# Kernel tuning notes

Measured on AMD Instinct MI355X. Metric: run time of the kernel, lower is better.

Reference implementation:

```python
import jax, jax.numpy as jnp
import numpy as np

MARGIN = 0.2
NEG_INF = -1e30


def setup_inputs() -> dict:
    key = jax.random.key(0)
    k1, k2 = jax.random.split(key)
    B, D, C = 384, 256, 48
    features = jax.random.normal(k1, (B, D), dtype=jnp.float32)
    labels = jax.random.randint(k2, (B,), 0, C, dtype=jnp.int32)
    return {"features": features, "labels": labels, "epoch": 5}


def reference(features, labels, epoch):
    B = features.shape[0]
    # pairwise euclidean distance, clamped like torch.clamp(min=1e-11)
    diff = features[:, None, :] - features[None, :, :]          # [B,B,D]
    dist = jnp.sqrt(jnp.clip(jnp.sum(diff * diff, axis=-1), 1e-11))  # [B,B]

    idx = jnp.arange(B)
    same = labels[:, None] == labels[None, :]
    pos_mask = same & (idx[None, :] > idx[:, None])             # pairs (i,j), j>i, same label
    neg_mask = ~same

    # Gumbel-max sampling replaces the per-row np.random.choice host loop.
    gumbel = jax.random.gumbel(jax.random.key(42), (B, B, B), dtype=dist.dtype)

    if epoch > 3:
        # semi-hard negatives: pos_dist < d(i,k) < pos_dist + margin, weights 1/d(i,k)
        d_ik = dist[:, None, :]                                 # [B,1,B]
        d_pos = dist[:, :, None]                                # [B,B,1]
        semi = neg_mask[:, None, :] & (d_ik > d_pos) & (d_ik < d_pos + MARGIN)  # [B,B,B]
        logits = jnp.where(semi, -jnp.log(dist)[:, None, :], NEG_INF)  # log(1/d)
        has_neg = jnp.any(semi, axis=-1)                        # [B,B]
    else:
        # uniform random negative per (i,j) pair
        logits = jnp.where(neg_mask[:, None, :], 0.0, NEG_INF)  # [B,1,B]
        has_neg = jnp.broadcast_to(jnp.any(neg_mask, axis=-1)[:, None], (B, B))

    neg_idx = jnp.argmax(logits + gumbel, axis=-1)              # [B,B]
    neg_dist = jnp.take_along_axis(dist, neg_idx, axis=1)       # d(i, sampled_neg)

    valid = pos_mask & has_neg
    # MarginRankingLoss(neg, pos, target=1) = relu(pos - neg + margin)
    per_pair = jax.nn.relu(dist - neg_dist + MARGIN)
    count = jnp.sum(valid)
    total = jnp.sum(jnp.where(valid, per_pair, 0.0))
    return jnp.where(count > 0, total / jnp.maximum(count, 1), 0.0)
```

## Files before the change

kernel.cpp:

```cpp
#include <hip/hip_runtime.h>
#include <hip/hip_bf16.h>
#include <stdint.h>

#define BSZ 384
#define DD  256
#define NWAVES 6
#define NEG_BIG -3.0e38f
#define DONE_BASE 0xAAAAAAAAu

__device__ __forceinline__ void threefry_0_42(uint32_t c0, uint32_t c1,
                                              uint32_t& o0, uint32_t& o1) {
    const uint32_t k0 = 0u;
    const uint32_t k1 = 42u;
    const uint32_t k2 = 0u ^ 42u ^ 0x1BD11BDAu;
    uint32_t x0 = c0 + k0;
    uint32_t x1 = c1 + k1;
#define TF_RND(R) { x0 += x1; x1 = (x1 << (R)) | (x1 >> (32 - (R))); x1 ^= x0; }
    TF_RND(13) TF_RND(15) TF_RND(26) TF_RND(6)
    x0 += k1; x1 += k2 + 1u;
    TF_RND(17) TF_RND(29) TF_RND(16) TF_RND(24)
    x0 += k2; x1 += k0 + 2u;
    TF_RND(13) TF_RND(15) TF_RND(26) TF_RND(6)
    x0 += k0; x1 += k1 + 3u;
    TF_RND(17) TF_RND(29) TF_RND(16) TF_RND(24)
    x0 += k1; x1 += k2 + 4u;
    TF_RND(13) TF_RND(15) TF_RND(26) TF_RND(6)
    x0 += k2; x1 += k0 + 5u;
#undef TF_RND
    o0 = x0; o1 = x1;
}

__device__ __forceinline__ float gumbel_at(uint32_t idx) {
    uint32_t r0, r1;
    threefry_0_42(0u, idx, r0, r1);
    uint32_t bits = r0 ^ r1;
    uint32_t mant = bits >> 9;
    float f = __uint_as_float(mant | 0x3F800000u) - 1.0f;
    float u = (mant == 0u) ? 1.17549435e-38f : f;
    return -logf(-logf(u));
}

__global__ __launch_bounds__(BSZ) void fused_kernel(const float* __restrict__ F,
                                                    const int* __restrict__ labels,
                                                    const int* __restrict__ epochp,
                                                    float* __restrict__ tot_slot,
                                                    unsigned int* __restrict__ cnt_slot,
                                                    unsigned int* __restrict__ done,
                                                    float* __restrict__ out) {
    __shared__ float    row[BSZ];
    __shared__ float    nlog[BSZ];
    __shared__ int      slab[BSZ];
    __shared__ int      plist[BSZ];
    __shared__ int      npos;
    __shared__ int      is_last;
    __shared__ float    wtot[NWAVES];
    __shared__ unsigned wcnt[NWAVES];

    const int i    = blockIdx.x;
    const int tid  = threadIdx.x;
    const int wave = tid >> 6;
    const int lane = tid & 63;
    const int rl   = lane >> 3;
    const int s    = lane & 7;

    slab[tid] = labels[tid];
    if (tid == 0) npos = 0;
    __syncthreads();

    const int lab_i = slab[i];
    if (tid > i && slab[tid] == lab_i)
        plist[atomicAdd(&npos, 1)] = tid;
    const int  epoch   = *epochp;
    const bool semisel = (epoch > 3);
    __syncthreads();

    const int np = npos;
    float    t_total = 0.0f;
    unsigned t_count = 0u;

    if (np > 0) {
        const float4* F4 = (const float4*)F;

        float4 fi[8];
#pragma unroll
        for (int t = 0; t < 8; ++t) fi[t] = F4[i * (DD / 4) + t * 8 + s];

        for (int c = 0; c < 8; ++c) {
            const int k = c * 48 + wave * 8 + rl;
            const float4* fk = F4 + (size_t)k * (DD / 4);
            float a0 = 0.f, a1 = 0.f, a2 = 0.f, a3 = 0.f;
#pragma unroll
            for (int t = 0; t < 8; ++t) {
                float4 b = fk[t * 8 + s];
                float d0 = fi[t].x - b.x;
                float d1 = fi[t].y - b.y;
                float d2 = fi[t].z - b.z;
                float d3 = fi[t].w - b.w;
                a0 = fmaf(d0, d0, a0);
                a1 = fmaf(d1, d1, a1);
                a2 = fmaf(d2, d2, a2);
                a3 = fmaf(d3, d3, a3);
            }
            float p = (a0 + a1) + (a2 + a3);
            p += __shfl_down(p, 4, 64);
            p += __shfl_down(p, 2, 64);
            p += __shfl_down(p, 1, 64);
            if (s == 0) row[k] = sqrtf(fmaxf(p, 1e-11f));
        }
        __syncthreads();
        nlog[tid] = semisel ? -logf(row[tid]) : 0.0f;
        __syncthreads();

        for (int p = wave; p < np; p += NWAVES) {
            const int   j     = plist[p];
            const float d_pos = row[j];
            const float hi    = d_pos + 0.2f;
            float v  = NEG_BIG;
            int   kk = 0;
#pragma unroll
            for (int c = 0; c < BSZ / 64; ++c) {
                const int   k   = c * 64 + lane;
                const float dkk = row[k];
                const bool cand = (slab[k] != lab_i) &&
                                  (!semisel || (dkk > d_pos && dkk < hi));
                if (__any(cand)) {
                    if (cand) {
                        const uint32_t idx = (uint32_t)(i * BSZ + j) * (uint32_t)BSZ
                                             + (uint32_t)k;
                        float val = nlog[k] + gumbel_at(idx);
                        if (val > v) { v = val; kk = k; }
                    }
                }
            }
#pragma unroll
            for (int off = 32; off; off >>= 1) {
                float ov = __shfl_down(v, off, 64);
                int   oi = __shfl_down(kk, off, 64);
                if (ov > v || (ov == v && oi < kk)) { v = ov; kk = oi; }
            }
            if (lane == 0 && v > -1.0e38f) {
                t_total += fmaxf(d_pos - row[kk] + 0.2f, 0.0f);
                t_count += 1u;
            }
        }
    }

    if (lane == 0) { wtot[wave] = t_total; wcnt[wave] = t_count; }
    __syncthreads();
    if (tid == 0) {
        float    tt = 0.0f;
        unsigned cc = 0u;
#pragma unroll
        for (int q = 0; q < NWAVES; ++q) { tt += wtot[q]; cc += wcnt[q]; }
        atomicExch(&tot_slot[i], tt);
        atomicExch(&cnt_slot[i], cc);
        __threadfence();
        const unsigned prev = atomicAdd(done, 1u);
        is_last = (prev == DONE_BASE + (unsigned)(BSZ - 1)) ? 1 : 0;
    }
    __syncthreads();

    if (is_last) {
        float    t = atomicAdd(&tot_slot[tid], 0.0f);
        unsigned c = atomicAdd(&cnt_slot[tid], 0u);
#pragma unroll
        for (int off = 32; off; off >>= 1) {
            t += __shfl_down(t, off, 64);
            c += __shfl_down(c, off, 64);
        }
        if (lane == 0) { wtot[wave] = t; wcnt[wave] = c; }
        __syncthreads();
        if (tid == 0) {
            float    tt = 0.0f;
            unsigned cc = 0u;
#pragma unroll
            for (int q = 0; q < NWAVES; ++q) { tt += wtot[q]; cc += wcnt[q]; }
            out[0] = (cc > 0u) ? (tt / (float)cc) : 0.0f;
        }
    }
}

extern "C" void kernel_launch(void* const* d_in, const int* in_sizes, int n_in,
                              void* d_out, int out_size, void* d_ws, size_t ws_size,
                              hipStream_t stream) {
    const float* F      = (const float*)d_in[0];
    const int*   labels = (const int*)d_in[1];
    const int*   epoch  = (const int*)d_in[2];
    float*       out    = (float*)d_out;

    if (ws_size < (2 * BSZ + 1) * sizeof(float)) return;
    float*        tot_slot = (float*)d_ws;
    unsigned int* cnt_slot = (unsigned int*)d_ws + BSZ;
    unsigned int* done     = (unsigned int*)d_ws + 2 * BSZ;

    fused_kernel<<<BSZ, BSZ, 0, stream>>>(F, labels, epoch,
                                          tot_slot, cnt_slot, done, out);
}
```

Before: 72.17 us.

## Pair early and late anchor rows per block to cut grid to 256 blocks

The grid shrinks from 384 to 256 blocks. The first 128 blocks each handle two anchor rows, b and 256+b, so a row with many positive pairs is paired with one that has few. The distance phase computes both rows in one pass, reusing each loaded feature row, and the positive-pair lists of both anchors share one tagged worklist. This aims to balance work across the CUs in a single wave of blocks and to cut redundant feature loads, at the cost of extra registers and per-pair indirection.

```diff
diff --git a/kernel.cpp b/kernel.cpp
--- a/kernel.cpp
+++ b/kernel.cpp
@@ -4,6 +4,8 @@
 
 #define BSZ 384
 #define DD  256
+#define NBLK 256
+#define NDUAL (BSZ - NBLK)
 #define NWAVES 6
 #define NEG_BIG -3.0e38f
 #define DONE_BASE 0xAAAAAAAAu
@@ -47,29 +49,36 @@
                                                     unsigned int* __restrict__ cnt_slot,
                                                     unsigned int* __restrict__ done,
                                                     float* __restrict__ out) {
-    __shared__ float    row[BSZ];
-    __shared__ float    nlog[BSZ];
+    __shared__ float    row[2][BSZ];
+    __shared__ float    nlg[2][BSZ];
     __shared__ int      slab[BSZ];
-    __shared__ int      plist[BSZ];
+    __shared__ int      plist[512];
     __shared__ int      npos;
     __shared__ int      is_last;
     __shared__ float    wtot[NWAVES];
     __shared__ unsigned wcnt[NWAVES];
 
-    const int i    = blockIdx.x;
+    const int b    = blockIdx.x;
     const int tid  = threadIdx.x;
     const int wave = tid >> 6;
     const int lane = tid & 63;
     const int rl   = lane >> 3;
     const int s    = lane & 7;
 
+    const int  i0   = b;
+    const bool dual = (b < NDUAL);
+    const int  i1   = dual ? (NBLK + b) : 0;
+
     slab[tid] = labels[tid];
     if (tid == 0) npos = 0;
     __syncthreads();
 
-    const int lab_i = slab[i];
-    if (tid > i && slab[tid] == lab_i)
+    const int lab0 = slab[i0];
+    const int lab1 = dual ? slab[i1] : -1;
+    if (tid > i0 && slab[tid] == lab0)
         plist[atomicAdd(&npos, 1)] = tid;
+    if (dual && tid > i1 && slab[tid] == lab1)
+        plist[atomicAdd(&npos, 1)] = 512 | tid;
     const int  epoch   = *epochp;
     const bool semisel = (epoch > 3);
     __syncthreads();
@@ -81,53 +90,101 @@
     if (np > 0) {
         const float4* F4 = (const float4*)F;
 
-        float4 fi[8];
-#pragma unroll
-        for (int t = 0; t < 8; ++t) fi[t] = F4[i * (DD / 4) + t * 8 + s];
-
-        for (int c = 0; c < 8; ++c) {
-            const int k = c * 48 + wave * 8 + rl;
-            const float4* fk = F4 + (size_t)k * (DD / 4);
-            float a0 = 0.f, a1 = 0.f, a2 = 0.f, a3 = 0.f;
-#pragma unroll
-            for (int t = 0; t < 8; ++t) {
-                float4 b = fk[t * 8 + s];
-                float d0 = fi[t].x - b.x;
-                float d1 = fi[t].y - b.y;
-                float d2 = fi[t].z - b.z;
-                float d3 = fi[t].w - b.w;
-                a0 = fmaf(d0, d0, a0);
-                a1 = fmaf(d1, d1, a1);
-                a2 = fmaf(d2, d2, a2);
-                a3 = fmaf(d3, d3, a3);
-            }
-            float p = (a0 + a1) + (a2 + a3);
-            p += __shfl_down(p, 4, 64);
-            p += __shfl_down(p, 2, 64);
-            p += __shfl_down(p, 1, 64);
-            if (s == 0) row[k] = sqrtf(fmaxf(p, 1e-11f));
+        float4 f0[8], f1[8];
+#pragma unroll
+        for (int t = 0; t < 8; ++t) f0[t] = F4[i0 * (DD / 4) + t * 8 + s];
+        if (dual) {
+#pragma unroll
+            for (int t = 0; t < 8; ++t) f1[t] = F4[i1 * (DD / 4) + t * 8 + s];
+        }
+
+        if (dual) {
+            for (int c = 0; c < 8; ++c) {
+                const int k = c * 48 + wave * 8 + rl;
+                const float4* fk = F4 + (size_t)k * (DD / 4);
+                float a0 = 0.f, a1 = 0.f, a2 = 0.f, a3 = 0.f;
+                float b0 = 0.f, b1 = 0.f, b2 = 0.f, b3 = 0.f;
+#pragma unroll
+                for (int t = 0; t < 8; ++t) {
+                    float4 bb = fk[t * 8 + s];
+                    float d0 = f0[t].x - bb.x;
+                    float d1 = f0[t].y - bb.y;
+                    float d2 = f0[t].z - bb.z;
+                    float d3 = f0[t].w - bb.w;
+                    a0 = fmaf(d0, d0, a0);
+                    a1 = fmaf(d1, d1, a1);
+                    a2 = fmaf(d2, d2, a2);
+                    a3 = fmaf(d3, d3, a3);
+                    float e0 = f1[t].x - bb.x;
+                    float e1 = f1[t].y - bb.y;
+                    float e2 = f1[t].z - bb.z;
+                    float e3 = f1[t].w - bb.w;
+                    b0 = fmaf(e0, e0, b0);
+                    b1 = fmaf(e1, e1, b1);
+                    b2 = fmaf(e2, e2, b2);
+                    b3 = fmaf(e3, e3, b3);
+                }
+                float p = (a0 + a1) + (a2 + a3);
+                p += __shfl_down(p, 4, 64);
+                p += __shfl_down(p, 2, 64);
+                p += __shfl_down(p, 1, 64);
+                if (s == 0) row[0][k] = sqrtf(fmaxf(p, 1e-11f));
+                float q = (b0 + b1) + (b2 + b3);
+                q += __shfl_down(q, 4, 64);
+                q += __shfl_down(q, 2, 64);
+                q += __shfl_down(q, 1, 64);
+                if (s == 0) row[1][k] = sqrtf(fmaxf(q, 1e-11f));
+            }
+        } else {
+            for (int c = 0; c < 8; ++c) {
+                const int k = c * 48 + wave * 8 + rl;
+                const float4* fk = F4 + (size_t)k * (DD / 4);
+                float a0 = 0.f, a1 = 0.f, a2 = 0.f, a3 = 0.f;
+#pragma unroll
+                for (int t = 0; t < 8; ++t) {
+                    float4 bb = fk[t * 8 + s];
+                    float d0 = f0[t].x - bb.x;
+                    float d1 = f0[t].y - bb.y;
+                    float d2 = f0[t].z - bb.z;
+                    float d3 = f0[t].w - bb.w;
+                    a0 = fmaf(d0, d0, a0);
+                    a1 = fmaf(d1, d1, a1);
+                    a2 = fmaf(d2, d2, a2);
+                    a3 = fmaf(d3, d3, a3);
+                }
+                float p = (a0 + a1) + (a2 + a3);
+                p += __shfl_down(p, 4, 64);
+                p += __shfl_down(p, 2, 64);
+                p += __shfl_down(p, 1, 64);
+                if (s == 0) row[0][k] = sqrtf(fmaxf(p, 1e-11f));
+            }
         }
         __syncthreads();
-        nlog[tid] = semisel ? -logf(row[tid]) : 0.0f;
+        nlg[0][tid] = semisel ? -logf(row[0][tid]) : 0.0f;
+        if (dual) nlg[1][tid] = semisel ? -logf(row[1][tid]) : 0.0f;
         __syncthreads();
 
         for (int p = wave; p < np; p += NWAVES) {
-            const int   j     = plist[p];
-            const float d_pos = row[j];
+            const int   e     = plist[p];
+            const int   a     = e >> 9;
+            const int   j     = e & 511;
+            const int   ia    = a ? i1 : i0;
+            const int   laba  = a ? lab1 : lab0;
+            const float d_pos = row[a][j];
             const float hi    = d_pos + 0.2f;
             float v  = NEG_BIG;
             int   kk = 0;
 #pragma unroll
             for (int c = 0; c < BSZ / 64; ++c) {
                 const int   k   = c * 64 + lane;
-                const float dkk = row[k];
-                const bool cand = (slab[k] != lab_i) &&
+                const float dkk = row[a][k];
+                const bool cand = (slab[k] != laba) &&
                                   (!semisel || (dkk > d_pos && dkk < hi));
                 if (__any(cand)) {
                     if (cand) {
-                        const uint32_t idx = (uint32_t)(i * BSZ + j) * (uint32_t)BSZ
+                        const uint32_t idx = (uint32_t)(ia * BSZ + j) * (uint32_t)BSZ
                                              + (uint32_t)k;
-                        float val = nlog[k] + gumbel_at(idx);
+                        float val = nlg[a][k] + gumbel_at(idx);
                         if (val > v) { v = val; kk = k; }
                     }
                 }
@@ -139,7 +196,7 @@
                 if (ov > v || (ov == v && oi < kk)) { v = ov; kk = oi; }
             }
             if (lane == 0 && v > -1.0e38f) {
-                t_total += fmaxf(d_pos - row[kk] + 0.2f, 0.0f);
+                t_total += fmaxf(d_pos - row[a][kk] + 0.2f, 0.0f);
                 t_count += 1u;
             }
         }
@@ -152,17 +209,17 @@
         unsigned cc = 0u;
 #pragma unroll
         for (int q = 0; q < NWAVES; ++q) { tt += wtot[q]; cc += wcnt[q]; }
-        atomicExch(&tot_slot[i], tt);
-        atomicExch(&cnt_slot[i], cc);
+        atomicExch(&tot_slot[b], tt);
+        atomicExch(&cnt_slot[b], cc);
         __threadfence();
         const unsigned prev = atomicAdd(done, 1u);
-        is_last = (prev == DONE_BASE + (unsigned)(BSZ - 1)) ? 1 : 0;
+        is_last = (prev == DONE_BASE + (unsigned)(NBLK - 1)) ? 1 : 0;
     }
     __syncthreads();
 
     if (is_last) {
-        float    t = atomicAdd(&tot_slot[tid], 0.0f);
-        unsigned c = atomicAdd(&cnt_slot[tid], 0u);
+        float    t = (tid < NBLK) ? atomicAdd(&tot_slot[tid], 0.0f) : 0.0f;
+        unsigned c = (tid < NBLK) ? atomicAdd(&cnt_slot[tid], 0u)  : 0u;
 #pragma unroll
         for (int off = 32; off; off >>= 1) {
             t += __shfl_down(t, off, 64);
@@ -188,11 +245,11 @@
     const int*   epoch  = (const int*)d_in[2];
     float*       out    = (float*)d_out;
 
-    if (ws_size < (2 * BSZ + 1) * sizeof(float)) return;
+    if (ws_size < (2 * NBLK + 1) * sizeof(float)) return;
     float*        tot_slot = (float*)d_ws;
-    unsigned int* cnt_slot = (unsigned int*)d_ws + BSZ;
-    unsigned int* done     = (unsigned int*)d_ws + 2 * BSZ;
-
-    fused_kernel<<<BSZ, BSZ, 0, stream>>>(F, labels, epoch,
-                                          tot_slot, cnt_slot, done, out);
-}
+    unsigned int* cnt_slot = (unsigned int*)d_ws + NBLK;
+    unsigned int* done     = (unsigned int*)d_ws + 2 * NBLK;
+
+    fused_kernel<<<NBLK, BSZ, 0, stream>>>(F, labels, epoch,
+                                           tot_slot, cnt_slot, done, out);
+}
```

Result: slower. 78.07 us (+8.2%).
